# Kernel tuning notes

Hardware: AMD Instinct MI355X
Metric: run time of the kernel (lower is better)

## Reference

```python
import jax, jax.numpy as jnp
import numpy as np

TOKENS = 2048
HIDDEN = 2048
INTER = 1408
EXPERTS = 16
TOP_K = 2


def setup_inputs() -> dict:
    key = jax.random.key(0)
    k_x, k_g, k_gp, k_up, k_dp = jax.random.split(key, 5)
    s = 0.02  # weight init scale
    return {
        "hidden_states": jax.random.normal(k_x, (TOKENS, HIDDEN), jnp.float32),
        "w_gate": jax.random.normal(k_g, (HIDDEN, EXPERTS), jnp.float32) * s,
        "w_gate_proj": jax.random.normal(k_gp, (EXPERTS, HIDDEN, INTER), jnp.float32) * s,
        "w_up_proj": jax.random.normal(k_up, (EXPERTS, HIDDEN, INTER), jnp.float32) * s,
        "w_down_proj": jax.random.normal(k_dp, (EXPERTS, INTER, HIDDEN), jnp.float32) * s,
    }


def reference(hidden_states, w_gate, w_gate_proj, w_up_proj, w_down_proj):
    T, H = hidden_states.shape
    E = w_gate.shape[1]
    # --- router: gate linear + top-k sigmoid routing (fused_topk_sigmoid) ---
    router_logits = hidden_states @ w_gate                      # [T, E]
    scores = jax.nn.sigmoid(router_logits.astype(jnp.float32))  # [T, E]
    topk_w, topk_ids = jax.lax.top_k(scores, TOP_K)             # [T, K]
    topk_w = topk_w / topk_w.sum(axis=-1, keepdims=True)        # renormalize (norm_topk_prob)
    # dense combine weights [T, E]: zero for unselected experts
    cw = jnp.zeros((T, E), jnp.float32).at[jnp.arange(T)[:, None], topk_ids].set(topk_w)
    # --- experts: SwiGLU MLP per expert, combined by routing weights ---
    g = jnp.einsum('th,ehi->eti', hidden_states, w_gate_proj)   # [E, T, I]
    u = jnp.einsum('th,ehi->eti', hidden_states, w_up_proj)     # [E, T, I]
    h = jax.nn.silu(g) * u                                      # [E, T, I]
    y = jnp.einsum('eti,eih->eth', h, w_down_proj)              # [E, T, H]
    out = jnp.einsum('eth,te->th', y, cw.astype(hidden_states.dtype))
    return out
```

## Files before the change

kernel.cpp:

```cpp
#include <hip/hip_runtime.h>
#include <stdint.h>

#define TOKENS 2048
#define HIDDEN 2048
#define INTER  1408
#define NEXP   16
#define LDA    40

using bf16x8 = __attribute__((ext_vector_type(8))) __bf16;
using f32x4  = __attribute__((ext_vector_type(4))) float;

__device__ __forceinline__ unsigned int bfround(float f) {
    union { float f; unsigned int u; } a; a.f = f;
    return (a.u + 0x7fffu + ((a.u >> 16) & 1u)) >> 16;
}
__device__ __forceinline__ unsigned int pack2(float a, float b) {
    return bfround(a) | (bfround(b) << 16);
}

__global__ __launch_bounds__(64) void router_kernel(
    const float* __restrict__ x, const float* __restrict__ wg,
    int* __restrict__ cnt, int* __restrict__ tok, float* __restrict__ wts)
{
    const int t = blockIdx.x;
    const int lane = threadIdx.x;
    float acc[NEXP];
#pragma unroll
    for (int e = 0; e < NEXP; e++) acc[e] = 0.f;
    const float* xr = x + (size_t)t * HIDDEN;
    for (int h = lane; h < HIDDEN; h += 64) {
        const float xv = xr[h];
        const float* wr = wg + (size_t)h * NEXP;
#pragma unroll
        for (int e = 0; e < NEXP; e++) acc[e] += xv * wr[e];
    }
#pragma unroll
    for (int off = 32; off > 0; off >>= 1) {
#pragma unroll
        for (int e = 0; e < NEXP; e++) acc[e] += __shfl_down(acc[e], off, 64);
    }
    if (lane == 0) {
        float s[NEXP];
#pragma unroll
        for (int e = 0; e < NEXP; e++) s[e] = 1.f / (1.f + __expf(-acc[e]));
        int i0 = 0;
#pragma unroll
        for (int e = 1; e < NEXP; e++) if (s[e] > s[i0]) i0 = e;
        int i1 = (i0 == 0) ? 1 : 0;
#pragma unroll
        for (int e = 0; e < NEXP; e++) if (e != i0 && s[e] > s[i1]) i1 = e;
        float w0 = s[i0], w1 = s[i1];
        const float inv = 1.f / (w0 + w1);
        w0 *= inv; w1 *= inv;
        const int s0 = atomicAdd(&cnt[i0], 1);
        tok[i0 * TOKENS + s0] = t * 2;
        wts[i0 * TOKENS + s0] = w0;
        const int s1 = atomicAdd(&cnt[i1], 1);
        tok[i1 * TOKENS + s1] = t * 2 + 1;
        wts[i1 * TOKENS + s1] = w1;
    }
}

__global__ __launch_bounds__(256) void gemm1_kernel(
    const float* __restrict__ x, const float* __restrict__ wgp,
    const float* __restrict__ wup, const int* __restrict__ cnt,
    const int* __restrict__ tok, unsigned short* __restrict__ hbuf)
{
    const int e = blockIdx.z;
    const int ne = cnt[e];
    const int m0 = blockIdx.y * 128;
    if (m0 >= ne) return;
    const int n0 = blockIdx.x * 64;

    __shared__ __align__(16) unsigned short As[128][LDA];
    __shared__ __align__(16) unsigned short Bs[2][64][LDA];
    __shared__ int rowp[128];

    const int tid = threadIdx.x;
    if (tid < 128) {
        const int slot = m0 + tid;
        const int cs = slot < ne ? slot : ne - 1;
        rowp[tid] = tok[e * TOKENS + cs];
    }
    __syncthreads();

    const int lane = tid & 63;
    const int wid  = tid >> 6;
    const int wm = (wid >> 1) * 64;
    const int wn = (wid & 1) * 32;
    const int lr = lane & 15;
    const int lq = lane >> 4;

    f32x4 accg[4][2], accu[4][2];
    const f32x4 z4 = {0.f, 0.f, 0.f, 0.f};
#pragma unroll
    for (int a = 0; a < 4; a++)
#pragma unroll
        for (int b = 0; b < 2; b++) { accg[a][b] = z4; accu[a][b] = z4; }

    const size_t wbase = (size_t)e * HIDDEN * INTER + n0;
    const float* wgq = wgp + wbase;
    const float* wuq = wup + wbase;

    const int arow = tid >> 3;
    const int acol = (tid & 7) * 4;
    int atok[4];
#pragma unroll
    for (int i = 0; i < 4; i++) atok[i] = rowp[arow + i * 32] >> 1;

    for (int k0 = 0; k0 < HIDDEN; k0 += 32) {
#pragma unroll
        for (int i = 0; i < 4; i++) {
            const float4 v = *(const float4*)(x + (size_t)atok[i] * HIDDEN + k0 + acol);
            uint2 pv; pv.x = pack2(v.x, v.y); pv.y = pack2(v.z, v.w);
            *(uint2*)&As[arow + i * 32][acol] = pv;
        }
#pragma unroll
        for (int i = 0; i < 4; i++) {
            const int sel = i >> 1;
            const int rem = ((i & 1) << 8) + tid;
            const int kg = rem >> 6;
            const int n  = rem & 63;
            const float* src = (sel ? wuq : wgq) + (size_t)(k0 + kg * 4) * INTER + n;
            uint2 pv;
            pv.x = pack2(src[0], src[(size_t)INTER]);
            pv.y = pack2(src[2 * (size_t)INTER], src[3 * (size_t)INTER]);
            *(uint2*)&Bs[sel][n][kg * 4] = pv;
        }
        __syncthreads();

        bf16x8 af[4], bg[2], bu[2];
#pragma unroll
        for (int tm = 0; tm < 4; tm++)
            af[tm] = *(const bf16x8*)&As[wm + tm * 16 + lr][lq * 8];
#pragma unroll
        for (int tn = 0; tn < 2; tn++) {
            bg[tn] = *(const bf16x8*)&Bs[0][wn + tn * 16 + lr][lq * 8];
            bu[tn] = *(const bf16x8*)&Bs[1][wn + tn * 16 + lr][lq * 8];
        }
#pragma unroll
        for (int tm = 0; tm < 4; tm++)
#pragma unroll
            for (int tn = 0; tn < 2; tn++) {
                accg[tm][tn] = __builtin_amdgcn_mfma_f32_16x16x32_bf16(af[tm], bg[tn], accg[tm][tn], 0, 0, 0);
                accu[tm][tn] = __builtin_amdgcn_mfma_f32_16x16x32_bf16(af[tm], bu[tn], accu[tm][tn], 0, 0, 0);
            }
        __syncthreads();
    }

#pragma unroll
    for (int tm = 0; tm < 4; tm++)
#pragma unroll
        for (int tn = 0; tn < 2; tn++)
#pragma unroll
            for (int r = 0; r < 4; r++) {
                const int rowL = wm + tm * 16 + lq * 4 + r;
                const int slot = m0 + rowL;
                if (slot < ne) {
                    const int p = rowp[rowL];
                    const int col = n0 + wn + tn * 16 + lr;
                    const float g = accg[tm][tn][r];
                    const float u = accu[tm][tn][r];
                    const float hv = g * u / (1.f + __expf(-g));
                    hbuf[(size_t)p * INTER + col] = (unsigned short)bfround(hv);
                }
            }
}

__global__ __launch_bounds__(256) void gemm2_kernel(
    const unsigned short* __restrict__ hbuf, const float* __restrict__ wdp,
    const int* __restrict__ cnt, const int* __restrict__ tok,
    const float* __restrict__ wts, float* __restrict__ out)
{
    const int e = blockIdx.z;
    const int ne = cnt[e];
    const int m0 = blockIdx.y * 128;
    if (m0 >= ne) return;
    const int n0 = blockIdx.x * 64;

    __shared__ __align__(16) unsigned short As[128][LDA];
    __shared__ __align__(16) unsigned short Bs[64][LDA];
    __shared__ int rowp[128];
    __shared__ float roww[128];

    const int tid = threadIdx.x;
    if (tid < 128) {
        const int slot = m0 + tid;
        const int cs = slot < ne ? slot : ne - 1;
        rowp[tid] = tok[e * TOKENS + cs];
        roww[tid] = wts[e * TOKENS + cs];
    }
    __syncthreads();

    const int lane = tid & 63;
    const int wid  = tid >> 6;
    const int wm = (wid >> 1) * 64;
    const int wn = (wid & 1) * 32;
    const int lr = lane & 15;
    const int lq = lane >> 4;

    f32x4 acc[4][2];
    const f32x4 z4 = {0.f, 0.f, 0.f, 0.f};
#pragma unroll
    for (int a = 0; a < 4; a++)
#pragma unroll
        for (int b = 0; b < 2; b++) acc[a][b] = z4;

    const float* wdq = wdp + (size_t)e * INTER * HIDDEN + n0;

    const int arow = tid >> 2;
    const int ac8  = (tid & 3) * 8;
    int ap[2];
    ap[0] = rowp[arow];
    ap[1] = rowp[arow + 64];

    for (int k0 = 0; k0 < INTER; k0 += 32) {
#pragma unroll
        for (int i = 0; i < 2; i++) {
            const uint4 v = *(const uint4*)(hbuf + (size_t)ap[i] * INTER + k0 + ac8);
            *(uint4*)&As[arow + i * 64][ac8] = v;
        }
#pragma unroll
        for (int i = 0; i < 2; i++) {
            const int sid = (i << 8) + tid;
            const int kg = sid >> 6;
            const int n  = sid & 63;
            const float* src = wdq + (size_t)(k0 + kg * 4) * HIDDEN + n;
            uint2 pv;
            pv.x = pack2(src[0], src[(size_t)HIDDEN]);
            pv.y = pack2(src[2 * (size_t)HIDDEN], src[3 * (size_t)HIDDEN]);
            *(uint2*)&Bs[n][kg * 4] = pv;
        }
        __syncthreads();

        bf16x8 af[4], bb[2];
#pragma unroll
        for (int tm = 0; tm < 4; tm++)
            af[tm] = *(const bf16x8*)&As[wm + tm * 16 + lr][lq * 8];
#pragma unroll
        for (int tn = 0; tn < 2; tn++)
            bb[tn] = *(const bf16x8*)&Bs[wn + tn * 16 + lr][lq * 8];
#pragma unroll
        for (int tm = 0; tm < 4; tm++)
#pragma unroll
            for (int tn = 0; tn < 2; tn++)
                acc[tm][tn] = __builtin_amdgcn_mfma_f32_16x16x32_bf16(af[tm], bb[tn], acc[tm][tn], 0, 0, 0);
        __syncthreads();
    }

#pragma unroll
    for (int tm = 0; tm < 4; tm++)
#pragma unroll
        for (int tn = 0; tn < 2; tn++)
#pragma unroll
            for (int r = 0; r < 4; r++) {
                const int rowL = wm + tm * 16 + lq * 4 + r;
                const int slot = m0 + rowL;
                if (slot < ne) {
                    const int t = rowp[rowL] >> 1;
                    const float w = roww[rowL];
                    atomicAdd(&out[(size_t)t * HIDDEN + n0 + wn + tn * 16 + lr],
                              w * acc[tm][tn][r]);
                }
            }
}

extern "C" void kernel_launch(void* const* d_in, const int* in_sizes, int n_in,
                              void* d_out, int out_size, void* d_ws, size_t ws_size,
                              hipStream_t stream) {
    const float* x   = (const float*)d_in[0];
    const float* wg  = (const float*)d_in[1];
    const float* wgp = (const float*)d_in[2];
    const float* wup = (const float*)d_in[3];
    const float* wdp = (const float*)d_in[4];
    float* out = (float*)d_out;

    char* ws = (char*)d_ws;
    int*   cnt  = (int*)ws;
    int*   tok  = (int*)(ws + 256);
    float* wts  = (float*)(ws + 256 + 131072);
    unsigned short* hbuf = (unsigned short*)(ws + 256 + 2 * 131072);

    hipMemsetAsync(cnt, 0, NEXP * sizeof(int), stream);
    hipMemsetAsync(out, 0, (size_t)TOKENS * HIDDEN * sizeof(float), stream);

    router_kernel<<<dim3(TOKENS), dim3(64), 0, stream>>>(x, wg, cnt, tok, wts);

    dim3 g1(INTER / 64, TOKENS / 128, NEXP);
    gemm1_kernel<<<g1, dim3(256), 0, stream>>>(x, wgp, wup, cnt, tok, hbuf);

    dim3 g2(HIDDEN / 64, TOKENS / 128, NEXP);
    gemm2_kernel<<<g2, dim3(256), 0, stream>>>(hbuf, wdp, cnt, tok, wts, out);
}
```

Before: 754.0 us.

## Prefetch next K tile into registers, widen BK to 64, swizzle LDS

The router kernel now also writes a bf16 copy of the activations, so gemm1 streams bf16 A rows instead of converting fp32 on every tile. Both GEMMs move to BK=64 with XOR-swizzled LDS rows in place of padding. Global loads for the next tile are issued into registers before the MFMA work on the current tile, giving software pipelining. Weight loads are reorganised so each lane gathers 8 consecutive K values and packs them with native bf16 conversion, at the cost of more registers and extra workspace for the bf16 activations.

After: 924.0 us. 1.23x slower.

```diff
diff --git a/kernel.cpp b/kernel.cpp
--- a/kernel.cpp
+++ b/kernel.cpp
@@ -5,22 +5,29 @@
 #define HIDDEN 2048
 #define INTER  1408
 #define NEXP   16
-#define LDA    40
+#define BK     64
+#define ROWU   64
 
 using bf16x8 = __attribute__((ext_vector_type(8))) __bf16;
 using f32x4  = __attribute__((ext_vector_type(4))) float;
 
-__device__ __forceinline__ unsigned int bfround(float f) {
-    union { float f; unsigned int u; } a; a.f = f;
-    return (a.u + 0x7fffu + ((a.u >> 16) & 1u)) >> 16;
-}
-__device__ __forceinline__ unsigned int pack2(float a, float b) {
-    return bfround(a) | (bfround(b) << 16);
+__device__ __forceinline__ unsigned short bf16bits(float f) {
+    union { __bf16 h; unsigned short u; } cv;
+    cv.h = (__bf16)f;
+    return cv.u;
+}
+
+__device__ __forceinline__ void pack8(const float* s, void* dst) {
+    bf16x8 v;
+#pragma unroll
+    for (int j = 0; j < 8; j++) v[j] = (__bf16)s[j];
+    *(bf16x8*)dst = v;
 }
 
 __global__ __launch_bounds__(64) void router_kernel(
     const float* __restrict__ x, const float* __restrict__ wg,
-    int* __restrict__ cnt, int* __restrict__ tok, float* __restrict__ wts)
+    int* __restrict__ cnt, int* __restrict__ tok, float* __restrict__ wts,
+    unsigned short* __restrict__ xbf)
 {
     const int t = blockIdx.x;
     const int lane = threadIdx.x;
@@ -28,8 +35,10 @@
 #pragma unroll
     for (int e = 0; e < NEXP; e++) acc[e] = 0.f;
     const float* xr = x + (size_t)t * HIDDEN;
+    unsigned short* xbr = xbf + (size_t)t * HIDDEN;
     for (int h = lane; h < HIDDEN; h += 64) {
         const float xv = xr[h];
+        xbr[h] = bf16bits(xv);
         const float* wr = wg + (size_t)h * NEXP;
 #pragma unroll
         for (int e = 0; e < NEXP; e++) acc[e] += xv * wr[e];
@@ -62,7 +71,7 @@
 }
 
 __global__ __launch_bounds__(256) void gemm1_kernel(
-    const float* __restrict__ x, const float* __restrict__ wgp,
+    const unsigned short* __restrict__ xbf, const float* __restrict__ wgp,
     const float* __restrict__ wup, const int* __restrict__ cnt,
     const int* __restrict__ tok, unsigned short* __restrict__ hbuf)
 {
@@ -72,15 +81,14 @@
     if (m0 >= ne) return;
     const int n0 = blockIdx.x * 64;
 
-    __shared__ __align__(16) unsigned short As[128][LDA];
-    __shared__ __align__(16) unsigned short Bs[2][64][LDA];
+    __shared__ __align__(16) unsigned short As[128 * ROWU];
+    __shared__ __align__(16) unsigned short Bs[2][64 * ROWU];
     __shared__ int rowp[128];
 
     const int tid = threadIdx.x;
     if (tid < 128) {
         const int slot = m0 + tid;
-        const int cs = slot < ne ? slot : ne - 1;
-        rowp[tid] = tok[e * TOKENS + cs];
+        rowp[tid] = tok[e * TOKENS + (slot < ne ? slot : ne - 1)];
     }
     __syncthreads();
 
@@ -91,6 +99,18 @@
     const int lr = lane & 15;
     const int lq = lane >> 4;
 
+    const int ar = tid >> 3;
+    const int ac = tid & 7;
+    const int apx = ac ^ (ar & 7);
+    const unsigned short* aptr[4];
+#pragma unroll
+    for (int i = 0; i < 4; i++)
+        aptr[i] = xbf + (size_t)(rowp[ar + i * 32] >> 1) * HIDDEN + ac * 8;
+
+    const float* bptr[2];
+    bptr[0] = wgp + (size_t)e * HIDDEN * INTER + n0 + lane;
+    bptr[1] = wup + (size_t)e * HIDDEN * INTER + n0 + lane;
+
     f32x4 accg[4][2], accu[4][2];
     const f32x4 z4 = {0.f, 0.f, 0.f, 0.f};
 #pragma unroll
@@ -98,53 +118,58 @@
 #pragma unroll
         for (int b = 0; b < 2; b++) { accg[a][b] = z4; accu[a][b] = z4; }
 
-    const size_t wbase = (size_t)e * HIDDEN * INTER + n0;
-    const float* wgq = wgp + wbase;
-    const float* wuq = wup + wbase;
-
-    const int arow = tid >> 3;
-    const int acol = (tid & 7) * 4;
-    int atok[4];
-#pragma unroll
-    for (int i = 0; i < 4; i++) atok[i] = rowp[arow + i * 32] >> 1;
-
-    for (int k0 = 0; k0 < HIDDEN; k0 += 32) {
-#pragma unroll
-        for (int i = 0; i < 4; i++) {
-            const float4 v = *(const float4*)(x + (size_t)atok[i] * HIDDEN + k0 + acol);
-            uint2 pv; pv.x = pack2(v.x, v.y); pv.y = pack2(v.z, v.w);
-            *(uint2*)&As[arow + i * 32][acol] = pv;
+    uint4 pa[4];
+    float pb[2][2][8];
+
+    auto loadAB = [&](int k0) {
+#pragma unroll
+        for (int i = 0; i < 4; i++) pa[i] = *(const uint4*)(aptr[i] + k0);
+#pragma unroll
+        for (int m = 0; m < 2; m++)
+#pragma unroll
+            for (int i = 0; i < 2; i++) {
+                const int c = i * 4 + wid;
+                const float* src = bptr[m] + (size_t)(k0 + c * 8) * INTER;
+#pragma unroll
+                for (int j = 0; j < 8; j++) pb[m][i][j] = src[(size_t)j * INTER];
+            }
+    };
+
+    loadAB(0);
+    for (int k0 = 0; k0 < HIDDEN; k0 += BK) {
+#pragma unroll
+        for (int i = 0; i < 4; i++)
+            *(uint4*)&As[(ar + i * 32) * ROWU + apx * 8] = pa[i];
+#pragma unroll
+        for (int m = 0; m < 2; m++)
+#pragma unroll
+            for (int i = 0; i < 2; i++) {
+                const int c = i * 4 + wid;
+                pack8(pb[m][i], &Bs[m][lane * ROWU + (c ^ (lane & 7)) * 8]);
+            }
+        __syncthreads();
+        if (k0 + BK < HIDDEN) loadAB(k0 + BK);
+
+#pragma unroll
+        for (int ks = 0; ks < 2; ks++) {
+            bf16x8 af[4], bg[2], bu[2];
+#pragma unroll
+            for (int tm = 0; tm < 4; tm++)
+                af[tm] = *(const bf16x8*)&As[(wm + tm * 16 + lr) * ROWU + ((ks * 4 + lq) ^ (lr & 7)) * 8];
+#pragma unroll
+            for (int tn = 0; tn < 2; tn++) {
+                const int off = (wn + tn * 16 + lr) * ROWU + ((ks * 4 + lq) ^ (lr & 7)) * 8;
+                bg[tn] = *(const bf16x8*)&Bs[0][off];
+                bu[tn] = *(const bf16x8*)&Bs[1][off];
+            }
+#pragma unroll
+            for (int tm = 0; tm < 4; tm++)
+#pragma unroll
+                for (int tn = 0; tn < 2; tn++) {
+                    accg[tm][tn] = __builtin_amdgcn_mfma_f32_16x16x32_bf16(af[tm], bg[tn], accg[tm][tn], 0, 0, 0);
+                    accu[tm][tn] = __builtin_amdgcn_mfma_f32_16x16x32_bf16(af[tm], bu[tn], accu[tm][tn], 0, 0, 0);
+                }
         }
-#pragma unroll
-        for (int i = 0; i < 4; i++) {
-            const int sel = i >> 1;
-            const int rem = ((i & 1) << 8) + tid;
-            const int kg = rem >> 6;
-            const int n  = rem & 63;
-            const float* src = (sel ? wuq : wgq) + (size_t)(k0 + kg * 4) * INTER + n;
-            uint2 pv;
-            pv.x = pack2(src[0], src[(size_t)INTER]);
-            pv.y = pack2(src[2 * (size_t)INTER], src[3 * (size_t)INTER]);
-            *(uint2*)&Bs[sel][n][kg * 4] = pv;
-        }
-        __syncthreads();
-
-        bf16x8 af[4], bg[2], bu[2];
-#pragma unroll
-        for (int tm = 0; tm < 4; tm++)
-            af[tm] = *(const bf16x8*)&As[wm + tm * 16 + lr][lq * 8];
-#pragma unroll
-        for (int tn = 0; tn < 2; tn++) {
-            bg[tn] = *(const bf16x8*)&Bs[0][wn + tn * 16 + lr][lq * 8];
-            bu[tn] = *(const bf16x8*)&Bs[1][wn + tn * 16 + lr][lq * 8];
-        }
-#pragma unroll
-        for (int tm = 0; tm < 4; tm++)
-#pragma unroll
-            for (int tn = 0; tn < 2; tn++) {
-                accg[tm][tn] = __builtin_amdgcn_mfma_f32_16x16x32_bf16(af[tm], bg[tn], accg[tm][tn], 0, 0, 0);
-                accu[tm][tn] = __builtin_amdgcn_mfma_f32_16x16x32_bf16(af[tm], bu[tn], accu[tm][tn], 0, 0, 0);
-            }
         __syncthreads();
     }
 
@@ -162,7 +187,7 @@
                     const float g = accg[tm][tn][r];
                     const float u = accu[tm][tn][r];
                     const float hv = g * u / (1.f + __expf(-g));
-                    hbuf[(size_t)p * INTER + col] = (unsigned short)bfround(hv);
+                    hbuf[(size_t)p * INTER + col] = bf16bits(hv);
                 }
             }
 }
@@ -178,8 +203,8 @@
     if (m0 >= ne) return;
     const int n0 = blockIdx.x * 64;
 
-    __shared__ __align__(16) unsigned short As[128][LDA];
-    __shared__ __align__(16) unsigned short Bs[64][LDA];
+    __shared__ __align__(16) unsigned short As[128 * ROWU];
+    __shared__ __align__(16) unsigned short Bs[64 * ROWU];
     __shared__ int rowp[128];
     __shared__ float roww[128];
 
@@ -199,6 +224,16 @@
     const int lr = lane & 15;
     const int lq = lane >> 4;
 
+    const int ar = tid >> 3;
+    const int ac = tid & 7;
+    const int apx = ac ^ (ar & 7);
+    const unsigned short* aptr[4];
+#pragma unroll
+    for (int i = 0; i < 4; i++)
+        aptr[i] = hbuf + (size_t)rowp[ar + i * 32] * INTER + ac * 8;
+
+    const float* bptr = wdp + (size_t)e * INTER * HIDDEN + n0 + lane;
+
     f32x4 acc[4][2];
     const f32x4 z4 = {0.f, 0.f, 0.f, 0.f};
 #pragma unroll
@@ -206,45 +241,49 @@
 #pragma unroll
         for (int b = 0; b < 2; b++) acc[a][b] = z4;
 
-    const float* wdq = wdp + (size_t)e * INTER * HIDDEN + n0;
-
-    const int arow = tid >> 2;
-    const int ac8  = (tid & 3) * 8;
-    int ap[2];
-    ap[0] = rowp[arow];
-    ap[1] = rowp[arow + 64];
-
-    for (int k0 = 0; k0 < INTER; k0 += 32) {
+    uint4 pa[4];
+    float pb[2][8];
+
+    auto loadAB = [&](int k0) {
+#pragma unroll
+        for (int i = 0; i < 4; i++) pa[i] = *(const uint4*)(aptr[i] + k0);
 #pragma unroll
         for (int i = 0; i < 2; i++) {
-            const uint4 v = *(const uint4*)(hbuf + (size_t)ap[i] * INTER + k0 + ac8);
-            *(uint4*)&As[arow + i * 64][ac8] = v;
+            const int c = i * 4 + wid;
+            const float* src = bptr + (size_t)(k0 + c * 8) * HIDDEN;
+#pragma unroll
+            for (int j = 0; j < 8; j++) pb[i][j] = src[(size_t)j * HIDDEN];
         }
+    };
+
+    loadAB(0);
+    for (int k0 = 0; k0 < INTER; k0 += BK) {
+#pragma unroll
+        for (int i = 0; i < 4; i++)
+            *(uint4*)&As[(ar + i * 32) * ROWU + apx * 8] = pa[i];
 #pragma unroll
         for (int i = 0; i < 2; i++) {
-            const int sid = (i << 8) + tid;
-            const int kg = sid >> 6;
-            const int n  = sid & 63;
-            const float* src = wdq + (size_t)(k0 + kg * 4) * HIDDEN + n;
-            uint2 pv;
-            pv.x = pack2(src[0], src[(size_t)HIDDEN]);
-            pv.y = pack2(src[2 * (size_t)HIDDEN], src[3 * (size_t)HIDDEN]);
-            *(uint2*)&Bs[n][kg * 4] = pv;
+            const int c = i * 4 + wid;
+            pack8(pb[i], &Bs[lane * ROWU + (c ^ (lane & 7)) * 8]);
         }
         __syncthreads();
-
-        bf16x8 af[4], bb[2];
-#pragma unroll
-        for (int tm = 0; tm < 4; tm++)
-            af[tm] = *(const bf16x8*)&As[wm + tm * 16 + lr][lq * 8];
-#pragma unroll
-        for (int tn = 0; tn < 2; tn++)
-            bb[tn] = *(const bf16x8*)&Bs[wn + tn * 16 + lr][lq * 8];
-#pragma unroll
-        for (int tm = 0; tm < 4; tm++)
+        if (k0 + BK < INTER) loadAB(k0 + BK);
+
+#pragma unroll
+        for (int ks = 0; ks < 2; ks++) {
+            bf16x8 af[4], bb[2];
+#pragma unroll
+            for (int tm = 0; tm < 4; tm++)
+                af[tm] = *(const bf16x8*)&As[(wm + tm * 16 + lr) * ROWU + ((ks * 4 + lq) ^ (lr & 7)) * 8];
 #pragma unroll
             for (int tn = 0; tn < 2; tn++)
-                acc[tm][tn] = __builtin_amdgcn_mfma_f32_16x16x32_bf16(af[tm], bb[tn], acc[tm][tn], 0, 0, 0);
+                bb[tn] = *(const bf16x8*)&Bs[(wn + tn * 16 + lr) * ROWU + ((ks * 4 + lq) ^ (lr & 7)) * 8];
+#pragma unroll
+            for (int tm = 0; tm < 4; tm++)
+#pragma unroll
+                for (int tn = 0; tn < 2; tn++)
+                    acc[tm][tn] = __builtin_amdgcn_mfma_f32_16x16x32_bf16(af[tm], bb[tn], acc[tm][tn], 0, 0, 0);
+        }
         __syncthreads();
     }
 
@@ -279,15 +318,16 @@
     int*   cnt  = (int*)ws;
     int*   tok  = (int*)(ws + 256);
     float* wts  = (float*)(ws + 256 + 131072);
-    unsigned short* hbuf = (unsigned short*)(ws + 256 + 2 * 131072);
+    unsigned short* xbf  = (unsigned short*)(ws + 262400);
+    unsigned short* hbuf = (unsigned short*)(ws + 262400 + 8388608);
 
     hipMemsetAsync(cnt, 0, NEXP * sizeof(int), stream);
     hipMemsetAsync(out, 0, (size_t)TOKENS * HIDDEN * sizeof(float), stream);
 
-    router_kernel<<<dim3(TOKENS), dim3(64), 0, stream>>>(x, wg, cnt, tok, wts);
+    router_kernel<<<dim3(TOKENS), dim3(64), 0, stream>>>(x, wg, cnt, tok, wts, xbf);
 
     dim3 g1(INTER / 64, TOKENS / 128, NEXP);
-    gemm1_kernel<<<g1, dim3(256), 0, stream>>>(x, wgp, wup, cnt, tok, hbuf);
+    gemm1_kernel<<<g1, dim3(256), 0, stream>>>(xbf, wgp, wup, cnt, tok, hbuf);
 
     dim3 g2(HIDDEN / 64, TOKENS / 128, NEXP);
     gemm2_kernel<<<g2, dim3(256), 0, stream>>>(hbuf, wdp, cnt, tok, wts, out);
```
